# Optimization experiments

Hardware: AMD Instinct MI355X
Metric: run time of the kernel (lower is better)

## Reference

```python
import jax, jax.numpy as jnp
import numpy as np

B, C, H, W = 8, 256, 64, 64
CK = 64  # C // k with k=4


def setup_inputs() -> dict:
    key = jax.random.key(0)
    ks = jax.random.split(key, 5)
    s = 1.0 / np.sqrt(C)
    return {
        "x": jax.random.normal(ks[0], (B, C, H, W), dtype=jnp.float32),
        "wq": jax.random.normal(ks[1], (CK, C), dtype=jnp.float32) * s,
        "bq": jnp.zeros((CK,), dtype=jnp.float32),
        "wk": jax.random.normal(ks[2], (CK, C), dtype=jnp.float32) * s,
        "bk": jnp.zeros((CK,), dtype=jnp.float32),
        "wv": jax.random.normal(ks[3], (C, C), dtype=jnp.float32) * s,
        "bv": jnp.zeros((C,), dtype=jnp.float32),
        "wg": jax.random.normal(ks[4], (C, C), dtype=jnp.float32) * s,
        "bg": jnp.zeros((C,), dtype=jnp.float32),
    }


def reference(x, wq, bq, wk, bk, wv, bv, wg, bg):
    b, c, h, w = x.shape
    n = h * w
    xf = x.reshape(b, c, n)  # [B, C, N]
    # 1x1 convs are channel-wise matmuls
    q = jnp.einsum('oc,bcn->bon', wq, xf) + bq[None, :, None]  # [B, Ck, N]
    k = jnp.einsum('oc,bcn->bon', wk, xf) + bk[None, :, None]  # [B, Ck, N]
    v = jnp.einsum('oc,bcn->bon', wv, xf) + bv[None, :, None]  # [B, C, N]
    # energy[b,i,j] = q[b,:,i] . k[b,:,j]
    energy = jnp.einsum('bci,bcj->bij', q, k)  # [B, N, N]
    energy = jax.nn.elu(energy) / n
    out = jnp.einsum('bcn,bnj->bcj', v, energy).reshape(b, c, h, w)
    out = jnp.einsum('oc,bchw->bohw', wg, out) + bg[None, :, None, None]
    return out
```

## Files before the change

kernel.cpp:

```cpp
#include <hip/hip_runtime.h>
#include <math.h>

#define BATCH 8
#define CH    256
#define NPIX  4096
#define CKDIM 64

typedef __attribute__((ext_vector_type(8))) short short8;
typedef __attribute__((ext_vector_type(4))) float f32x4;

#define MFMA16x16(a, b, c) __builtin_amdgcn_mfma_f32_16x16x32_bf16((a), (b), (c), 0, 0, 0)

__device__ __forceinline__ unsigned short f2bf(float f) {
    union { float f; unsigned int u; } v; v.f = f;
    unsigned int u = v.u;
    u += 0x7fffu + ((u >> 16) & 1u);
    return (unsigned short)(u >> 16);
}

__global__ void prep_kernel(const float* __restrict__ wq, const float* __restrict__ bq,
                            const float* __restrict__ wk, const float* __restrict__ bk,
                            const float* __restrict__ wv, const float* __restrict__ bv,
                            const float* __restrict__ wg,
                            unsigned short* __restrict__ W_all, float* __restrict__ bias_all) {
    int bo  = blockIdx.x;
    int tid = threadIdx.x;
    if (bo < 16) {
        int r0 = bo * 8;
#pragma unroll
        for (int r = 0; r < 8; ++r) {
            int o = r0 + r;
            float v = (o < 64) ? wq[o * CH + tid] : wk[(o - 64) * CH + tid];
            W_all[o * CH + tid] = f2bf(v);
        }
        if (tid < 8) {
            int o = r0 + tid;
            bias_all[o] = (o < 64) ? bq[o] : bk[o - 64];
        }
    } else {
        int ob = (bo - 16) * 8;
        __shared__ float wgl[8][256];
#pragma unroll
        for (int r = 0; r < 8; ++r) wgl[r][tid] = wg[(size_t)(ob + r) * CH + tid];
        __syncthreads();
        float acc[8];
#pragma unroll
        for (int r = 0; r < 8; ++r) acc[r] = 0.f;
        for (int m = 0; m < CH; ++m) {
            float wvv = wv[(size_t)m * CH + tid];
#pragma unroll
            for (int r = 0; r < 8; ++r) acc[r] += wgl[r][m] * wvv;
        }
#pragma unroll
        for (int r = 0; r < 8; ++r)
            W_all[(size_t)(128 + ob + r) * CH + tid] = f2bf(acc[r]);
        if (tid < 8) {
            float bb = 0.f;
            for (int m = 0; m < CH; ++m) bb += wgl[tid][m] * bv[m];
            bias_all[128 + ob + tid] = bb;
        }
    }
}

__global__ void xpose_kernel(const float* __restrict__ x, unsigned short* __restrict__ xt) {
    __shared__ float Tl[64][65];
    int n0 = blockIdx.x * 64;
    int c0 = blockIdx.y * 64;
    int b  = blockIdx.z;
    int tid = threadIdx.x;

#pragma unroll
    for (int r = 0; r < 4; ++r) {
        int f  = r * 256 + tid;
        int c  = f >> 4;
        int n4 = f & 15;
        float4 v = *(const float4*)(x + ((size_t)b * CH + c0 + c) * NPIX + n0 + n4 * 4);
        Tl[n4 * 4 + 0][c] = v.x;
        Tl[n4 * 4 + 1][c] = v.y;
        Tl[n4 * 4 + 2][c] = v.z;
        Tl[n4 * 4 + 3][c] = v.w;
    }
    __syncthreads();
#pragma unroll
    for (int r = 0; r < 2; ++r) {
        int f    = r * 256 + tid;
        int nrow = f >> 3;
        int c8   = f & 7;
        unsigned int pk[4];
#pragma unroll
        for (int p = 0; p < 4; ++p) {
            unsigned int lo = f2bf(Tl[nrow][c8 * 8 + p * 2 + 0]);
            unsigned int hi = f2bf(Tl[nrow][c8 * 8 + p * 2 + 1]);
            pk[p] = lo | (hi << 16);
        }
        *(uint4*)(xt + ((size_t)b * NPIX + n0 + nrow) * CH + c0 + c8 * 8) = *(uint4*)pk;
    }
}

__global__ void qkv_mfma(const unsigned short* __restrict__ xt,
                         const unsigned short* __restrict__ W_all,
                         const float* __restrict__ bias_all,
                         unsigned short* __restrict__ qg, unsigned short* __restrict__ kg,
                         unsigned short* __restrict__ vp) {
    __shared__ __align__(16) unsigned short Xl[64][264];

    int n0   = blockIdx.x * 64;
    int b    = blockIdx.y;
    int tid  = threadIdx.x;
    int lane = tid & 63;
    int w    = tid >> 6;
    int col  = lane & 15;
    int quad = lane >> 4;

#pragma unroll
    for (int r = 0; r < 8; ++r) {
        int f   = r * 256 + tid;
        int row = f >> 5;
        int c8  = f & 31;
        *(uint4*)&Xl[row][c8 * 8] = *(const uint4*)(xt + ((size_t)b * NPIX + n0 + row) * CH + c8 * 8);
    }
    __syncthreads();

#pragma unroll
    for (int og = 0; og < 6; ++og) {
        int o0 = og * 64;
        const unsigned short* Arow = W_all + (size_t)(o0 + w * 16 + col) * CH + quad * 8;

        f32x4 acc[4];
#pragma unroll
        for (int t = 0; t < 4; ++t) acc[t] = (f32x4){0.f, 0.f, 0.f, 0.f};

#pragma unroll
        for (int kc = 0; kc < 8; ++kc) {
            short8 a = *(const short8*)(Arow + kc * 32);
#pragma unroll
            for (int nt = 0; nt < 4; ++nt) {
                short8 bb = *(const short8*)&Xl[nt * 16 + col][kc * 32 + quad * 8];
                acc[nt] = MFMA16x16(a, bb, acc[nt]);
            }
        }

        float4 bias = *(const float4*)(bias_all + o0 + w * 16 + quad * 4);
        float bs[4] = {bias.x, bias.y, bias.z, bias.w};

        if (og < 2) {
            unsigned short* dst = (og == 0) ? qg : kg;
#pragma unroll
            for (int nt = 0; nt < 4; ++nt) {
                int n = n0 + nt * 16 + col;
                unsigned int pk[2];
#pragma unroll
                for (int p = 0; p < 2; ++p) {
                    unsigned int lo = f2bf(acc[nt][p * 2 + 0] + bs[p * 2 + 0]);
                    unsigned int hi = f2bf(acc[nt][p * 2 + 1] + bs[p * 2 + 1]);
                    pk[p] = lo | (hi << 16);
                }
                *(uint2*)(dst + ((size_t)b * NPIX + n) * 64 + w * 16 + quad * 4) = *(uint2*)pk;
            }
        } else {
#pragma unroll
            for (int nt = 0; nt < 4; ++nt) {
                int n = n0 + nt * 16 + col;
#pragma unroll
                for (int r = 0; r < 4; ++r) {
                    int oo = o0 - 128 + w * 16 + quad * 4 + r;
                    vp[((size_t)b * CH + oo) * NPIX + n] = f2bf(acc[nt][r] + bs[r]);
                }
            }
        }
    }
}

#define LQ 72
__global__ __launch_bounds__(512, 4)
void attn_v6(const unsigned short* __restrict__ qg,
             const unsigned short* __restrict__ kg,
             const unsigned short* __restrict__ vp,
             const float* __restrict__ bg, float* __restrict__ out) {
    __shared__ __align__(16) unsigned short Qt[2][64][LQ];
    __shared__ __align__(16) unsigned short St[2][64][LQ];

    int j0   = blockIdx.x * 64;
    int b    = blockIdx.y;
    int tid  = threadIdx.x;
    int lane = tid & 63;
    int w    = tid >> 6;
    int col  = lane & 15;
    int quad = lane >> 4;

    int tiw = w >> 1;
    int tjh = w & 1;

    const size_t nb = (size_t)b * NPIX;
    int srow = tid >> 3, sq8 = tid & 7;

    short8 bK[2][2];
#pragma unroll
    for (int tjl = 0; tjl < 2; ++tjl)
#pragma unroll
        for (int ks = 0; ks < 2; ++ks)
            bK[tjl][ks] = *(const short8*)(kg + (nb + j0 + (tjh * 2 + tjl) * 16 + col) * 64 + ks * 32 + quad * 8);

    *(uint4*)&Qt[0][srow][sq8 * 8] = *(const uint4*)(qg + (nb + srow) * 64 + sq8 * 8);

    f32x4 acc[2][4];
#pragma unroll
    for (int ot = 0; ot < 2; ++ot)
#pragma unroll
        for (int tj = 0; tj < 4; ++tj) acc[ot][tj] = (f32x4){0.f, 0.f, 0.f, 0.f};

    __syncthreads();

    uint4 qn = *(const uint4*)(qg + (nb + 64 + srow) * 64 + sq8 * 8);
    {
        short8 aq0 = *(const short8*)&Qt[0][tiw * 16 + col][quad * 8];
        short8 aq1 = *(const short8*)&Qt[0][tiw * 16 + col][32 + quad * 8];
#pragma unroll
        for (int tjl = 0; tjl < 2; ++tjl) {
            f32x4 s = (f32x4){0.f, 0.f, 0.f, 0.f};
            s = MFMA16x16(aq0, bK[tjl][0], s);
            s = MFMA16x16(aq1, bK[tjl][1], s);
            unsigned int pk[2];
#pragma unroll
            for (int p = 0; p < 2; ++p) {
                float e0 = s[p * 2 + 0], e1 = s[p * 2 + 1];
                e0 = (e0 > 0.f) ? e0 : (__expf(e0) - 1.f);
                e1 = (e1 > 0.f) ? e1 : (__expf(e1) - 1.f);
                e0 *= (1.f / (float)NPIX);
                e1 *= (1.f / (float)NPIX);
                pk[p] = (unsigned int)f2bf(e0) | ((unsigned int)f2bf(e1) << 16);
            }
            *(uint2*)&St[0][(tjh * 2 + tjl) * 16 + col][tiw * 16 + quad * 4] = *(uint2*)pk;
        }
    }
    *(uint4*)&Qt[1][srow][sq8 * 8] = qn;
    uint4 aV[2][2];
#pragma unroll
    for (int ot = 0; ot < 2; ++ot)
#pragma unroll
        for (int ks = 0; ks < 2; ++ks)
            aV[ot][ks] = *(const uint4*)(vp + ((size_t)b * CH + (2 * w + ot) * 16 + col) * NPIX + ks * 32 + quad * 8);
    __syncthreads();

    for (int t = 1; t < 64; ++t) {
        int i0 = t * 64;
        int p  = t & 1;
        uint4 q2 = *(const uint4*)(qg + (nb + (((t + 1) & 63) * 64) + srow) * 64 + sq8 * 8);

        short8 aq0 = *(const short8*)&Qt[p][tiw * 16 + col][quad * 8];
        short8 aq1 = *(const short8*)&Qt[p][tiw * 16 + col][32 + quad * 8];
#pragma unroll
        for (int tjl = 0; tjl < 2; ++tjl) {
            f32x4 s = (f32x4){0.f, 0.f, 0.f, 0.f};
            s = MFMA16x16(aq0, bK[tjl][0], s);
            s = MFMA16x16(aq1, bK[tjl][1], s);
            unsigned int pk[2];
#pragma unroll
            for (int pp = 0; pp < 2; ++pp) {
                float e0 = s[pp * 2 + 0], e1 = s[pp * 2 + 1];
                e0 = (e0 > 0.f) ? e0 : (__expf(e0) - 1.f);
                e1 = (e1 > 0.f) ? e1 : (__expf(e1) - 1.f);
                e0 *= (1.f / (float)NPIX);
                e1 *= (1.f / (float)NPIX);
                pk[pp] = (unsigned int)f2bf(e0) | ((unsigned int)f2bf(e1) << 16);
            }
            *(uint2*)&St[p][(tjh * 2 + tjl) * 16 + col][tiw * 16 + quad * 4] = *(uint2*)pk;
        }
        *(uint4*)&Qt[p ^ 1][srow][sq8 * 8] = q2;

#pragma unroll
        for (int ks = 0; ks < 2; ++ks) {
            short8 sb[4];
#pragma unroll
            for (int tj = 0; tj < 4; ++tj)
                sb[tj] = *(const short8*)&St[p ^ 1][tj * 16 + col][ks * 32 + quad * 8];
#pragma unroll
            for (int ot = 0; ot < 2; ++ot)
#pragma unroll
                for (int tj = 0; tj < 4; ++tj)
                    acc[ot][tj] = MFMA16x16(sb[tj], *(const short8*)&aV[ot][ks], acc[ot][tj]);
        }
#pragma unroll
        for (int ot = 0; ot < 2; ++ot)
#pragma unroll
            for (int ks = 0; ks < 2; ++ks)
                aV[ot][ks] = *(const uint4*)(vp + ((size_t)b * CH + (2 * w + ot) * 16 + col) * NPIX + i0 + ks * 32 + quad * 8);
        __syncthreads();
    }

#pragma unroll
    for (int ks = 0; ks < 2; ++ks) {
        short8 sb[4];
#pragma unroll
        for (int tj = 0; tj < 4; ++tj)
            sb[tj] = *(const short8*)&St[1][tj * 16 + col][ks * 32 + quad * 8];
#pragma unroll
        for (int ot = 0; ot < 2; ++ot)
#pragma unroll
            for (int tj = 0; tj < 4; ++tj)
                acc[ot][tj] = MFMA16x16(sb[tj], *(const short8*)&aV[ot][ks], acc[ot][tj]);
    }

#pragma unroll
    for (int ot = 0; ot < 2; ++ot) {
        int o = (w * 2 + ot) * 16 + col;
        float bgv = bg[o];
#pragma unroll
        for (int tj = 0; tj < 4; ++tj) {
            int j = j0 + tj * 16 + quad * 4;
            float4 st;
            st.x = acc[ot][tj][0] + bgv;
            st.y = acc[ot][tj][1] + bgv;
            st.z = acc[ot][tj][2] + bgv;
            st.w = acc[ot][tj][3] + bgv;
            *(float4*)&out[((size_t)b * CH + o) * NPIX + j] = st;
        }
    }
}

extern "C" void kernel_launch(void* const* d_in, const int* in_sizes, int n_in,
                              void* d_out, int out_size, void* d_ws, size_t ws_size,
                              hipStream_t stream) {
    const float* x  = (const float*)d_in[0];
    const float* wq = (const float*)d_in[1];
    const float* bq = (const float*)d_in[2];
    const float* wk = (const float*)d_in[3];
    const float* bk = (const float*)d_in[4];
    const float* wv = (const float*)d_in[5];
    const float* bv = (const float*)d_in[6];
    const float* wg = (const float*)d_in[7];
    const float* bg = (const float*)d_in[8];
    float* out = (float*)d_out;

    unsigned short* W_all = (unsigned short*)d_ws;
    float* bias_all = (float*)(W_all + 384 * 256);
    unsigned short* xt = (unsigned short*)(bias_all + 384);
    unsigned short* qg = xt + (size_t)BATCH * NPIX * CH;
    unsigned short* kg = qg + (size_t)BATCH * NPIX * 64;
    unsigned short* vp = kg + (size_t)BATCH * NPIX * 64;

    prep_kernel<<<dim3(48), dim3(256), 0, stream>>>(wq, bq, wk, bk, wv, bv, wg, W_all, bias_all);
    xpose_kernel<<<dim3(NPIX / 64, CH / 64, BATCH), dim3(256), 0, stream>>>(x, xt);
    qkv_mfma<<<dim3(NPIX / 64, BATCH), dim3(256), 0, stream>>>(xt, W_all, bias_all, qg, kg, vp);
    attn_v6<<<dim3(NPIX / 64, BATCH), dim3(512), 0, stream>>>(qg, kg, vp, bg, out);
}
```

Baseline: 274.9 us.

## Retile attention warps, load Q directly into registers, split QKV grid by output group

The attention kernel drops the shared-memory Q staging buffer and has each warp load its Q fragment straight from global memory into registers. The energy-times-V stage is remapped so each warp covers 64 output channels by 32 columns instead of 32 by 64. That halves the shared-memory S fragment reads per warp but doubles the V registers per warp. The QKV projection grid gains a third dimension that splits the six output groups across three blocks to raise parallelism, at the cost of reloading the X tile three times. A cheaper bf16 pack (round-half-up instead of round-to-even) is used for the energy values.

```diff
diff --git a/kernel.cpp b/kernel.cpp
--- a/kernel.cpp
+++ b/kernel.cpp
@@ -4,7 +4,6 @@
 #define BATCH 8
 #define CH    256
 #define NPIX  4096
-#define CKDIM 64
 
 typedef __attribute__((ext_vector_type(8))) short short8;
 typedef __attribute__((ext_vector_type(4))) float f32x4;
@@ -16,6 +15,10 @@
     unsigned int u = v.u;
     u += 0x7fffu + ((u >> 16) & 1u);
     return (unsigned short)(u >> 16);
+}
+__device__ __forceinline__ unsigned int pack_bf2(float a, float b) {
+    union { float f; unsigned int u; } x, y; x.f = a; y.f = b;
+    return ((x.u + 0x8000u) >> 16) | ((y.u + 0x8000u) & 0xffff0000u);
 }
 
 __global__ void prep_kernel(const float* __restrict__ wq, const float* __restrict__ bq,
@@ -88,11 +91,9 @@
         int c8   = f & 7;
         unsigned int pk[4];
 #pragma unroll
-        for (int p = 0; p < 4; ++p) {
-            unsigned int lo = f2bf(Tl[nrow][c8 * 8 + p * 2 + 0]);
-            unsigned int hi = f2bf(Tl[nrow][c8 * 8 + p * 2 + 1]);
-            pk[p] = lo | (hi << 16);
-        }
+        for (int p = 0; p < 4; ++p)
+            pk[p] = (unsigned int)f2bf(Tl[nrow][c8 * 8 + p * 2 + 0]) |
+                    ((unsigned int)f2bf(Tl[nrow][c8 * 8 + p * 2 + 1]) << 16);
         *(uint4*)(xt + ((size_t)b * NPIX + n0 + nrow) * CH + c0 + c8 * 8) = *(uint4*)pk;
     }
 }
@@ -105,7 +106,8 @@
     __shared__ __align__(16) unsigned short Xl[64][264];
 
     int n0   = blockIdx.x * 64;
-    int b    = blockIdx.y;
+    int gsel = blockIdx.y;
+    int b    = blockIdx.z;
     int tid  = threadIdx.x;
     int lane = tid & 63;
     int w    = tid >> 6;
@@ -122,7 +124,8 @@
     __syncthreads();
 
 #pragma unroll
-    for (int og = 0; og < 6; ++og) {
+    for (int og2 = 0; og2 < 2; ++og2) {
+        int og = gsel * 2 + og2;
         int o0 = og * 64;
         const unsigned short* Arow = W_all + (size_t)(o0 + w * 16 + col) * CH + quad * 8;
 
@@ -150,11 +153,9 @@
                 int n = n0 + nt * 16 + col;
                 unsigned int pk[2];
 #pragma unroll
-                for (int p = 0; p < 2; ++p) {
-                    unsigned int lo = f2bf(acc[nt][p * 2 + 0] + bs[p * 2 + 0]);
-                    unsigned int hi = f2bf(acc[nt][p * 2 + 1] + bs[p * 2 + 1]);
-                    pk[p] = lo | (hi << 16);
-                }
+                for (int p = 0; p < 2; ++p)
+                    pk[p] = (unsigned int)f2bf(acc[nt][p * 2 + 0] + bs[p * 2 + 0]) |
+                            ((unsigned int)f2bf(acc[nt][p * 2 + 1] + bs[p * 2 + 1]) << 16);
                 *(uint2*)(dst + ((size_t)b * NPIX + n) * 64 + w * 16 + quad * 4) = *(uint2*)pk;
             }
         } else {
@@ -173,11 +174,10 @@
 
 #define LQ 72
 __global__ __launch_bounds__(512, 4)
-void attn_v6(const unsigned short* __restrict__ qg,
+void attn_v7(const unsigned short* __restrict__ qg,
              const unsigned short* __restrict__ kg,
              const unsigned short* __restrict__ vp,
              const float* __restrict__ bg, float* __restrict__ out) {
-    __shared__ __align__(16) unsigned short Qt[2][64][LQ];
     __shared__ __align__(16) unsigned short St[2][64][LQ];
 
     int j0   = blockIdx.x * 64;
@@ -190,124 +190,118 @@
 
     int tiw = w >> 1;
     int tjh = w & 1;
+    int wo  = w & 3;
+    int wjB = w >> 2;
 
     const size_t nb = (size_t)b * NPIX;
-    int srow = tid >> 3, sq8 = tid & 7;
 
     short8 bK[2][2];
 #pragma unroll
     for (int tjl = 0; tjl < 2; ++tjl)
 #pragma unroll
         for (int ks = 0; ks < 2; ++ks)
-            bK[tjl][ks] = *(const short8*)(kg + (nb + j0 + (tjh * 2 + tjl) * 16 + col) * 64 + ks * 32 + quad * 8);
-
-    *(uint4*)&Qt[0][srow][sq8 * 8] = *(const uint4*)(qg + (nb + srow) * 64 + sq8 * 8);
-
-    f32x4 acc[2][4];
-#pragma unroll
-    for (int ot = 0; ot < 2; ++ot)
-#pragma unroll
-        for (int tj = 0; tj < 4; ++tj) acc[ot][tj] = (f32x4){0.f, 0.f, 0.f, 0.f};
-
+            bK[tjl][ks] = *(const short8*)(kg + (nb + j0 + tjh * 32 + tjl * 16 + col) * 64 + ks * 32 + quad * 8);
+
+    const unsigned short* qbase = qg + (nb + tiw * 16 + col) * 64 + quad * 8;
+    const unsigned short* vbase = vp + ((size_t)b * CH + wo * 64 + col) * NPIX + quad * 8;
+
+    uint4 aq[2];
+#pragma unroll
+    for (int ks = 0; ks < 2; ++ks) aq[ks] = *(const uint4*)(qbase + ks * 32);
+    uint4 aV[4][2];
+#pragma unroll
+    for (int ot = 0; ot < 4; ++ot)
+#pragma unroll
+        for (int ks = 0; ks < 2; ++ks)
+            aV[ot][ks] = *(const uint4*)(vbase + (size_t)ot * 16 * NPIX + ks * 32);
+
+    f32x4 acc[4][2];
+#pragma unroll
+    for (int ot = 0; ot < 4; ++ot)
+#pragma unroll
+        for (int tj = 0; tj < 2; ++tj) acc[ot][tj] = (f32x4){0.f, 0.f, 0.f, 0.f};
+
+#pragma unroll
+    for (int tjl = 0; tjl < 2; ++tjl) {
+        f32x4 s = (f32x4){0.f, 0.f, 0.f, 0.f};
+        s = MFMA16x16(*(const short8*)&aq[0], bK[tjl][0], s);
+        s = MFMA16x16(*(const short8*)&aq[1], bK[tjl][1], s);
+        float e[4];
+#pragma unroll
+        for (int r = 0; r < 4; ++r) {
+            float v = s[r];
+            e[r] = ((v > 0.f) ? v : (__expf(v) - 1.f)) * (1.f / (float)NPIX);
+        }
+        unsigned int pk[2] = {pack_bf2(e[0], e[1]), pack_bf2(e[2], e[3])};
+        *(uint2*)&St[0][tjh * 32 + tjl * 16 + col][tiw * 16 + quad * 4] = *(uint2*)pk;
+    }
+#pragma unroll
+    for (int ks = 0; ks < 2; ++ks) aq[ks] = *(const uint4*)(qbase + 64 * 64 + ks * 32);
     __syncthreads();
 
-    uint4 qn = *(const uint4*)(qg + (nb + 64 + srow) * 64 + sq8 * 8);
-    {
-        short8 aq0 = *(const short8*)&Qt[0][tiw * 16 + col][quad * 8];
-        short8 aq1 = *(const short8*)&Qt[0][tiw * 16 + col][32 + quad * 8];
+#pragma unroll 2
+    for (int t = 1; t < 64; ++t) {
+        int p = t & 1;
 #pragma unroll
         for (int tjl = 0; tjl < 2; ++tjl) {
             f32x4 s = (f32x4){0.f, 0.f, 0.f, 0.f};
-            s = MFMA16x16(aq0, bK[tjl][0], s);
-            s = MFMA16x16(aq1, bK[tjl][1], s);
-            unsigned int pk[2];
-#pragma unroll
-            for (int p = 0; p < 2; ++p) {
-                float e0 = s[p * 2 + 0], e1 = s[p * 2 + 1];
-                e0 = (e0 > 0.f) ? e0 : (__expf(e0) - 1.f);
-                e1 = (e1 > 0.f) ? e1 : (__expf(e1) - 1.f);
-                e0 *= (1.f / (float)NPIX);
-                e1 *= (1.f / (float)NPIX);
-                pk[p] = (unsigned int)f2bf(e0) | ((unsigned int)f2bf(e1) << 16);
+            s = MFMA16x16(*(const short8*)&aq[0], bK[tjl][0], s);
+            s = MFMA16x16(*(const short8*)&aq[1], bK[tjl][1], s);
+            float e[4];
+#pragma unroll
+            for (int r = 0; r < 4; ++r) {
+                float v = s[r];
+                e[r] = ((v > 0.f) ? v : (__expf(v) - 1.f)) * (1.f / (float)NPIX);
             }
-            *(uint2*)&St[0][(tjh * 2 + tjl) * 16 + col][tiw * 16 + quad * 4] = *(uint2*)pk;
-        }
-    }
-    *(uint4*)&Qt[1][srow][sq8 * 8] = qn;
-    uint4 aV[2][2];
-#pragma unroll
-    for (int ot = 0; ot < 2; ++ot)
-#pragma unroll
-        for (int ks = 0; ks < 2; ++ks)
-            aV[ot][ks] = *(const uint4*)(vp + ((size_t)b * CH + (2 * w + ot) * 16 + col) * NPIX + ks * 32 + quad * 8);
-    __syncthreads();
-
-    for (int t = 1; t < 64; ++t) {
-        int i0 = t * 64;
-        int p  = t & 1;
-        uint4 q2 = *(const uint4*)(qg + (nb + (((t + 1) & 63) * 64) + srow) * 64 + sq8 * 8);
-
-        short8 aq0 = *(const short8*)&Qt[p][tiw * 16 + col][quad * 8];
-        short8 aq1 = *(const short8*)&Qt[p][tiw * 16 + col][32 + quad * 8];
-#pragma unroll
-        for (int tjl = 0; tjl < 2; ++tjl) {
-            f32x4 s = (f32x4){0.f, 0.f, 0.f, 0.f};
-            s = MFMA16x16(aq0, bK[tjl][0], s);
-            s = MFMA16x16(aq1, bK[tjl][1], s);
-            unsigned int pk[2];
-#pragma unroll
-            for (int pp = 0; pp < 2; ++pp) {
-                float e0 = s[pp * 2 + 0], e1 = s[pp * 2 + 1];
-                e0 = (e0 > 0.f) ? e0 : (__expf(e0) - 1.f);
-                e1 = (e1 > 0.f) ? e1 : (__expf(e1) - 1.f);
-                e0 *= (1.f / (float)NPIX);
-                e1 *= (1.f / (float)NPIX);
-                pk[pp] = (unsigned int)f2bf(e0) | ((unsigned int)f2bf(e1) << 16);
-            }
-            *(uint2*)&St[p][(tjh * 2 + tjl) * 16 + col][tiw * 16 + quad * 4] = *(uint2*)pk;
-        }
-        *(uint4*)&Qt[p ^ 1][srow][sq8 * 8] = q2;
-
+            unsigned int pk[2] = {pack_bf2(e[0], e[1]), pack_bf2(e[2], e[3])};
+            *(uint2*)&St[p][tjh * 32 + tjl * 16 + col][tiw * 16 + quad * 4] = *(uint2*)pk;
+        }
+        {
+            int inext = ((t + 1) & 63) * 64;
+#pragma unroll
+            for (int ks = 0; ks < 2; ++ks)
+                aq[ks] = *(const uint4*)(qbase + (size_t)inext * 64 + ks * 32);
+        }
 #pragma unroll
         for (int ks = 0; ks < 2; ++ks) {
-            short8 sb[4];
-#pragma unroll
-            for (int tj = 0; tj < 4; ++tj)
-                sb[tj] = *(const short8*)&St[p ^ 1][tj * 16 + col][ks * 32 + quad * 8];
-#pragma unroll
-            for (int ot = 0; ot < 2; ++ot)
-#pragma unroll
-                for (int tj = 0; tj < 4; ++tj)
+            short8 sb[2];
+#pragma unroll
+            for (int tj = 0; tj < 2; ++tj)
+                sb[tj] = *(const short8*)&St[p ^ 1][wjB * 32 + tj * 16 + col][ks * 32 + quad * 8];
+#pragma unroll
+            for (int ot = 0; ot < 4; ++ot)
+#pragma unroll
+                for (int tj = 0; tj < 2; ++tj)
                     acc[ot][tj] = MFMA16x16(sb[tj], *(const short8*)&aV[ot][ks], acc[ot][tj]);
         }
 #pragma unroll
-        for (int ot = 0; ot < 2; ++ot)
+        for (int ot = 0; ot < 4; ++ot)
 #pragma unroll
             for (int ks = 0; ks < 2; ++ks)
-                aV[ot][ks] = *(const uint4*)(vp + ((size_t)b * CH + (2 * w + ot) * 16 + col) * NPIX + i0 + ks * 32 + quad * 8);
+                aV[ot][ks] = *(const uint4*)(vbase + (size_t)ot * 16 * NPIX + t * 64 + ks * 32);
         __syncthreads();
     }
 
 #pragma unroll
     for (int ks = 0; ks < 2; ++ks) {
-        short8 sb[4];
-#pragma unroll
-        for (int tj = 0; tj < 4; ++tj)
-            sb[tj] = *(const short8*)&St[1][tj * 16 + col][ks * 32 + quad * 8];
-#pragma unroll
-        for (int ot = 0; ot < 2; ++ot)
-#pragma unroll
-            for (int tj = 0; tj < 4; ++tj)
+        short8 sb[2];
+#pragma unroll
+        for (int tj = 0; tj < 2; ++tj)
+            sb[tj] = *(const short8*)&St[1][wjB * 32 + tj * 16 + col][ks * 32 + quad * 8];
+#pragma unroll
+        for (int ot = 0; ot < 4; ++ot)
+#pragma unroll
+            for (int tj = 0; tj < 2; ++tj)
                 acc[ot][tj] = MFMA16x16(sb[tj], *(const short8*)&aV[ot][ks], acc[ot][tj]);
     }
 
 #pragma unroll
-    for (int ot = 0; ot < 2; ++ot) {
-        int o = (w * 2 + ot) * 16 + col;
+    for (int ot = 0; ot < 4; ++ot) {
+        int o = wo * 64 + ot * 16 + col;
         float bgv = bg[o];
 #pragma unroll
-        for (int tj = 0; tj < 4; ++tj) {
-            int j = j0 + tj * 16 + quad * 4;
+        for (int tj = 0; tj < 2; ++tj) {
+            int j = j0 + wjB * 32 + tj * 16 + quad * 4;
             float4 st;
             st.x = acc[ot][tj][0] + bgv;
             st.y = acc[ot][tj][1] + bgv;
@@ -341,6 +335,6 @@
 
     prep_kernel<<<dim3(48), dim3(256), 0, stream>>>(wq, bq, wk, bk, wv, bv, wg, W_all, bias_all);
     xpose_kernel<<<dim3(NPIX / 64, CH / 64, BATCH), dim3(256), 0, stream>>>(x, xt);
-    qkv_mfma<<<dim3(NPIX / 64, BATCH), dim3(256), 0, stream>>>(xt, W_all, bias_all, qg, kg, vp);
-    attn_v6<<<dim3(NPIX / 64, BATCH), dim3(512), 0, stream>>>(qg, kg, vp, bg, out);
-}
+    qkv_mfma<<<dim3(NPIX / 64, 3, BATCH), dim3(256), 0, stream>>>(xt, W_all, bias_all, qg, kg, vp);
+    attn_v7<<<dim3(NPIX / 64, BATCH), dim3(512), 0, stream>>>(qg, kg, vp, bg, out);
+}
```

After: 486.1 us. 1.77x slower.
